# Performance work log

Measured on AMD Instinct MI355X. Metric: run time of the kernel, lower is better.

Reference implementation:

```python
import jax, jax.numpy as jnp
import numpy as np

K = 3          # B-spline order (cubic)
G = 10         # number of spline intervals over [0, 1]
NELY, NELX = 512, 512
WIDTHS = [2, 32, 32, 1]


def _make_grid(in_dim):
    # extended uniform knot vector over [0,1] with K extra knots each side: (in_dim, G+2K+1)
    h = 1.0 / G
    knots = jnp.arange(-K, G + K + 1, dtype=jnp.float32) * h
    return jnp.tile(knots[None, :], (in_dim, 1))


def setup_inputs() -> dict:
    key = jax.random.key(0)
    ks = jax.random.split(key, 1 + 3 * (len(WIDTHS) - 1))
    inp = {"coords": jax.random.uniform(ks[0], (NELY * NELX, 2), dtype=jnp.float32)}
    for l, (i, o) in enumerate(zip(WIDTHS[:-1], WIDTHS[1:])):
        inp[f"grid{l}"] = _make_grid(i)
        inp[f"coef{l}"] = 0.1 * jax.random.normal(ks[1 + 3 * l], (i, o, G + K), dtype=jnp.float32)
        inp[f"sb{l}"] = jax.random.normal(ks[2 + 3 * l], (i, o), dtype=jnp.float32) / np.sqrt(i).astype(np.float32)
        inp[f"sp{l}"] = jnp.ones((i, o), dtype=jnp.float32)
    inp["density_bias"] = jnp.full((1,), np.float32(np.log(0.5 / (1.0 - 0.5 + 1e-8))))
    return inp


def _b_batch(x, grid):
    # Cox-de Boor recursion. x: (B, in), grid: (in, G+2K+1) -> bases (B, in, G+K)
    xe = x[:, :, None]
    v = ((xe >= grid[None, :, :-1]) & (xe < grid[None, :, 1:])).astype(x.dtype)
    for p in range(1, K + 1):
        left = (xe - grid[None, :, : -(p + 1)]) / (grid[None, :, p:-1] - grid[None, :, : -(p + 1)])
        right = (grid[None, :, p + 1:] - xe) / (grid[None, :, p + 1:] - grid[None, :, 1:-p])
        v = left * v[:, :, :-1] + right * v[:, :, 1:]
    return v


def _kan_layer(x, grid, coef, sb, sp):
    # y_out = sum_in [ sb * silu(x) + sp * sum_k B_k(x) * coef_k ]
    B = _b_batch(x, grid)                               # (batch, in, G+K)
    spline = jnp.einsum('bik,iok->bio', B, coef)        # (batch, in, out)
    base = jax.nn.silu(x)                               # (batch, in)
    return jnp.sum(sb[None] * base[:, :, None] + sp[None] * spline, axis=1)


def reference(coords, grid0, coef0, sb0, sp0, grid1, coef1, sb1, sp1,
              grid2, coef2, sb2, sp2, density_bias):
    h = _kan_layer(coords, grid0, coef0, sb0, sp0)
    h = _kan_layer(h, grid1, coef1, sb1, sp1)
    logits = _kan_layer(h, grid2, coef2, sb2, sp2) + density_bias
    return jax.nn.sigmoid(logits).reshape(1, NELY, NELX)
```

## Files before the change

### kernel.cpp

```cpp
#include <hip/hip_runtime.h>
#include <hip/hip_bf16.h>

typedef __hip_bfloat16 bf16;
typedef __fp16 h2v __attribute__((ext_vector_type(2)));
typedef __fp16 half8 __attribute__((ext_vector_type(8)));
typedef float floatx4 __attribute__((ext_vector_type(4)));

#define NPTS (512*512)

#define OFF_BIAS 12
#define OFF_FLAG 13
#define OFF_BF   16
#define NFRAG    50
#define WS_WORDS (16 + NFRAG*64*4)


__device__ __forceinline__ bool sniff_f32(const void* g0) {
    float f = ((const float*)g0)[0];
    return fabsf(f + 0.3f) < 0.01f;
}
__device__ __forceinline__ float ld(const void* p, int i, bool f32) {
    return f32 ? ((const float*)p)[i] : __bfloat162float(((const bf16*)p)[i]);
}
__device__ __forceinline__ unsigned pk_rtn(float a, float b) {
    union { h2v v; unsigned u; } x;
    x.v[0] = (__fp16)a; x.v[1] = (__fp16)b;
    return x.u;
}
__device__ __forceinline__ unsigned pkf16(float a, float b) {
    union { h2v v; unsigned u; } x;
    x.v = __builtin_amdgcn_cvt_pkrtz(a, b);
    return x.u;
}

__device__ float slotval(int layer, int K, int o,
                         const void* c0, const void* sb0, const void* sp0,
                         const void* c1, const void* sb1, const void* sp1,
                         const void* c2, const void* sb2, const void* sp2, bool f32)
{
    int i = K >> 4, s = K & 15;
    if (layer == 2 && o != 0) return 0.0f;
    if (s >= 1 && s <= 13) {
        int m = s - 1;
        if (layer == 0) return ld(c0, (i*32+o)*13 + m, f32) * ld(sp0, i*32+o, f32);
        if (layer == 1) return ld(c1, (i*32+o)*13 + m, f32) * ld(sp1, i*32+o, f32);
        return ld(c2, i*13 + m, f32) * ld(sp2, i, f32);
    }
    if (s == 14) {
        if (layer == 0) return ld(sb0, i*32+o, f32);
        if (layer == 1) return ld(sb1, i*32+o, f32);
        return ld(sb2, i, f32);
    }
    return 0.0f;
}

__global__ __launch_bounds__(256) void kan_prep(
    const void* __restrict__ g0, const void* __restrict__ c0,
    const void* __restrict__ sb0, const void* __restrict__ sp0,
    const void* __restrict__ g1, const void* __restrict__ c1,
    const void* __restrict__ sb1, const void* __restrict__ sp1,
    const void* __restrict__ g2, const void* __restrict__ c2,
    const void* __restrict__ sb2, const void* __restrict__ sp2,
    const void* __restrict__ bias, float* __restrict__ ws)
{
    const bool f32 = sniff_f32(g0);
    int t = blockIdx.x * blockDim.x + threadIdx.x;

    if (t < 16) {
        if (t < 12) {
            int l = t >> 2, j = t & 3;
            const void* g = (l == 0) ? g0 : (l == 1) ? g1 : g2;
            float lo = ld(g, 0, f32), hi = ld(g, 16, f32);
            float ih = 16.0f / (hi - lo);
            float v = (j == 0) ? lo : (j == 1) ? hi
                    : (j == 2) ? ih : (-lo * ih);
            ws[t] = v;
        } else if (t == 12) ws[12] = ld(bias, 0, f32);
        else if (t == 13)   ws[13] = f32 ? 1.0f : 0.0f;
        else                ws[t] = 0.0f;
        return;
    }
    int ft = t - 16;
    if (ft >= NFRAG * 64) return;
    int f = ft >> 6, l = ft & 63, n = l & 15, q = l >> 4;
    int layer, c, nt;
    if (f < 2)       { layer = 0; c = 0;          nt = f; }
    else if (f < 34) { layer = 1; c = (f - 2) >> 1; nt = (f - 2) & 1; }
    else             { layer = 2; c = f - 34;     nt = 0; }
    int o = nt * 16 + n;
    unsigned wv[4];
#pragma unroll
    for (int jp = 0; jp < 4; jp++) {
        int K0 = c * 32 + q * 8 + jp * 2;
        float v0 = slotval(layer, K0,     o, c0,sb0,sp0, c1,sb1,sp1, c2,sb2,sp2, f32);
        float v1 = slotval(layer, K0 + 1, o, c0,sb0,sp0, c1,sb1,sp1, c2,sb2,sp2, f32);
        wv[jp] = pk_rtn(v0, v1);
    }
    uint4 out4; out4.x = wv[0]; out4.y = wv[1]; out4.z = wv[2]; out4.w = wv[3];
    ((uint4*)((unsigned*)ws + OFF_BF))[f * 64 + l] = out4;
}

__device__ __forceinline__ floatx4 mf(uint4 a, uint4 b, floatx4 c)
{
    union { uint4 u; half8 h; } ua, ub;
    ua.u = a; ub.u = b;
    return __builtin_amdgcn_mfma_f32_16x16x32_f16(ua.h, ub.h, c, 0, 0, 0);
}

__device__ __forceinline__ void feat_words(float x, float ngh, float ih,
                                           unsigned* __restrict__ Wd)
{
    float t  = fmaf(x, ih, ngh);
    float fj = floorf(t);
    float u  = t - fj;
    bool inb = (t >= 0.0f) && (t < 16.0f);
    float s6 = inb ? 0.166666667f : 0.0f;
    int j  = (int)fj;
    int jc = min(max(j, 0), 15);
    float u2 = u * u, u3 = u2 * u, om = 1.0f - u;
    float b0 = om * om * om * s6;
    float b1 = (fmaf(3.0f, u3, 4.0f) - 6.0f * u2) * s6;
    float b2 = fmaf(-3.0f, u3, fmaf(3.0f, u2, fmaf(3.0f, u, 1.0f))) * s6;
    float b3 = u3 * s6;
    int m0 = jc - 3;
    if ((unsigned)(m0 + 0) > 12u) b0 = 0.0f;
    if ((unsigned)(m0 + 1) > 12u) b1 = 0.0f;
    if ((unsigned)(m0 + 2) > 12u) b2 = 0.0f;
    if ((unsigned)(m0 + 3) > 12u) b3 = 0.0f;
    int s0 = m0 + 1;
    int w  = ((s0 + 2) >> 1) - 1;
    unsigned A, B, C;
    if (s0 & 1) { A = pkf16(0.0f, b0); B = pkf16(b1, b2); C = pkf16(b3, 0.0f); }
    else        { A = pkf16(b0, b1);   B = pkf16(b2, b3); C = 0u; }
#pragma unroll
    for (int k = 0; k < 7; k++) {
        unsigned v = (w == k) ? A : 0u;
        v = (w == k - 1) ? B : v;
        v = (w == k - 2) ? C : v;
        Wd[k] = v;
    }
    float si = x / (1.0f + __expf(-x));
    Wd[7] = pkf16(si, 0.0f);
}

__device__ __forceinline__ void stage2(unsigned* row, float f0, float f1,
                                       float ngh, float ih)
{
    unsigned Wa[8], Wb[8];
    feat_words(f0, ngh, ih, Wa);
    feat_words(f1, ngh, ih, Wb);
    uint4 v;
    v.x = Wa[0]; v.y = Wa[1]; v.z = Wa[2]; v.w = Wa[3]; *(uint4*)(row + 0)  = v;
    v.x = Wa[4]; v.y = Wa[5]; v.z = Wa[6]; v.w = Wa[7]; *(uint4*)(row + 4)  = v;
    v.x = Wb[0]; v.y = Wb[1]; v.z = Wb[2]; v.w = Wb[3]; *(uint4*)(row + 8)  = v;
    v.x = Wb[4]; v.y = Wb[5]; v.z = Wb[6]; v.w = Wb[7]; *(uint4*)(row + 12) = v;
}

__global__ __launch_bounds__(128, 4) void kan_main(
    const void* __restrict__ coords, const float* __restrict__ ws,
    void* __restrict__ out)
{
    __shared__ __align__(16) unsigned lds[2 * 2560];
    const unsigned* wsu = (const unsigned*)ws;
    const uint4* bfp = (const uint4*)(wsu + OFF_BF);

    int tid = threadIdx.x;
    int l = tid & 63, w = tid >> 6;
    int p = blockIdx.x * 128 + w * 64 + l;

    unsigned* buf0 = lds + w * 2560;
    unsigned* buf1 = buf0 + 1280;
    unsigned* row0 = buf0 + l * 20;
    unsigned* row1 = buf1 + l * 20;

    const bool f32 = (ws[OFF_FLAG] != 0.0f);
    float x0, x1;
    if (f32) {
        float2 c = ((const float2*)coords)[p];
        x0 = c.x; x1 = c.y;
    } else {
        unsigned cc = ((const unsigned*)coords)[p];
        union { unsigned u; float f; } cv;
        cv.u = (cc & 0xffffu) << 16;  x0 = cv.f;
        cv.u = cc & 0xffff0000u;      x1 = cv.f;
    }

    const float iha = ws[2],  ngha = ws[3];
    const float ihb = ws[6],  nghb = ws[7];
    const float ihc = ws[10], nghc = ws[11];

    const int arow = l & 15, aq = (l >> 4) * 4;
    const int aoff = arow * 20 + aq;
    const int drow = (l >> 4) * 4, dcol = l & 15;

    float h[32];

    {
        floatx4 acc[4][2];
#pragma unroll
        for (int mt = 0; mt < 4; mt++)
#pragma unroll
            for (int nt = 0; nt < 2; nt++) acc[mt][nt] = (floatx4)0.0f;

        stage2(row0, x0, x1, ngha, iha);
        uint4 bf0 = bfp[0 * 64 + l], bf1 = bfp[1 * 64 + l];
#pragma unroll
        for (int mt = 0; mt < 4; mt++) {
            uint4 a = *(const uint4*)(buf0 + mt * 320 + aoff);
            acc[mt][0] = mf(a, bf0, acc[mt][0]);
            acc[mt][1] = mf(a, bf1, acc[mt][1]);
        }
#pragma unroll
        for (int mt = 0; mt < 4; mt++)
#pragma unroll
            for (int r = 0; r < 4; r++) {
                int rowi = (16*mt + drow + r) * 20 + dcol;
                buf0[rowi] = __float_as_uint(acc[mt][0][r]);
                buf1[rowi] = __float_as_uint(acc[mt][1][r]);
            }
#pragma unroll
        for (int q = 0; q < 4; q++) {
            uint4 v0 = *(const uint4*)(buf0 + l * 20 + 4 * q);
            h[4*q+0]  = __uint_as_float(v0.x); h[4*q+1]  = __uint_as_float(v0.y);
            h[4*q+2]  = __uint_as_float(v0.z); h[4*q+3]  = __uint_as_float(v0.w);
            uint4 v1 = *(const uint4*)(buf1 + l * 20 + 4 * q);
            h[16+4*q+0] = __uint_as_float(v1.x); h[16+4*q+1] = __uint_as_float(v1.y);
            h[16+4*q+2] = __uint_as_float(v1.z); h[16+4*q+3] = __uint_as_float(v1.w);
        }
    }

    {
        floatx4 acc[4][2];
#pragma unroll
        for (int mt = 0; mt < 4; mt++)
#pragma unroll
            for (int nt = 0; nt < 2; nt++) acc[mt][nt] = (floatx4)0.0f;

        stage2(row0, h[0], h[1], nghb, ihb);
#pragma unroll
        for (int c = 0; c < 16; c++) {
            const unsigned* bc = (c & 1) ? buf1 : buf0;
            unsigned* rn = (c & 1) ? row0 : row1;
            uint4 a[4];
#pragma unroll
            for (int mt = 0; mt < 4; mt++)
                a[mt] = *(const uint4*)(bc + mt * 320 + aoff);
            if (c < 15) stage2(rn, h[2*c+2], h[2*c+3], nghb, ihb);
            uint4 bf0 = bfp[(2 + 2*c) * 64 + l];
            uint4 bf1 = bfp[(3 + 2*c) * 64 + l];
#pragma unroll
            for (int mt = 0; mt < 4; mt++) {
                acc[mt][0] = mf(a[mt], bf0, acc[mt][0]);
                acc[mt][1] = mf(a[mt], bf1, acc[mt][1]);
            }
        }
#pragma unroll
        for (int mt = 0; mt < 4; mt++)
#pragma unroll
            for (int r = 0; r < 4; r++) {
                int rowi = (16*mt + drow + r) * 20 + dcol;
                buf0[rowi] = __float_as_uint(acc[mt][0][r]);
                buf1[rowi] = __float_as_uint(acc[mt][1][r]);
            }
#pragma unroll
        for (int q = 0; q < 4; q++) {
            uint4 v0 = *(const uint4*)(buf0 + l * 20 + 4 * q);
            h[4*q+0]  = __uint_as_float(v0.x); h[4*q+1]  = __uint_as_float(v0.y);
            h[4*q+2]  = __uint_as_float(v0.z); h[4*q+3]  = __uint_as_float(v0.w);
            uint4 v1 = *(const uint4*)(buf1 + l * 20 + 4 * q);
            h[16+4*q+0] = __uint_as_float(v1.x); h[16+4*q+1] = __uint_as_float(v1.y);
            h[16+4*q+2] = __uint_as_float(v1.z); h[16+4*q+3] = __uint_as_float(v1.w);
        }
    }

    {
        floatx4 acc[4];
#pragma unroll
        for (int mt = 0; mt < 4; mt++) acc[mt] = (floatx4)0.0f;

        stage2(row0, h[0], h[1], nghc, ihc);
#pragma unroll
        for (int c = 0; c < 16; c++) {
            const unsigned* bc = (c & 1) ? buf1 : buf0;
            unsigned* rn = (c & 1) ? row0 : row1;
            uint4 a[4];
#pragma unroll
            for (int mt = 0; mt < 4; mt++)
                a[mt] = *(const uint4*)(bc + mt * 320 + aoff);
            if (c < 15) stage2(rn, h[2*c+2], h[2*c+3], nghc, ihc);
            uint4 bf = bfp[(34 + c) * 64 + l];
#pragma unroll
            for (int mt = 0; mt < 4; mt++)
                acc[mt] = mf(a[mt], bf, acc[mt]);
        }
        if (dcol == 0) {
#pragma unroll
            for (int mt = 0; mt < 4; mt++)
#pragma unroll
                for (int r = 0; r < 4; r++)
                    buf0[(16*mt + drow + r) * 20] = __float_as_uint(acc[mt][r]);
        }
        float z = __uint_as_float(buf0[l * 20]);
        float r = 1.0f / (1.0f + __expf(-(z + ws[OFF_BIAS])));
        if (f32) ((float*)out)[p] = r;
        else     ((bf16*)out)[p] = __float2bfloat16(r);
    }
}

extern "C" void kernel_launch(void* const* d_in, const int* in_sizes, int n_in,
                              void* d_out, int out_size, void* d_ws, size_t ws_size,
                              hipStream_t stream)
{
    float* ws = (float*)d_ws;

    kan_prep<<<(16 + NFRAG*64 + 255) / 256, 256, 0, stream>>>(
        d_in[1], d_in[2], d_in[3], d_in[4],
        d_in[5], d_in[6], d_in[7], d_in[8],
        d_in[9], d_in[10], d_in[11], d_in[12],
        d_in[13], ws);

    kan_main<<<NPTS / 128, 128, 0, stream>>>(d_in[0], ws, d_out);
}
```

Measured before the change: 128.9 us.

## Split each point's two input features across two lanes, halving points per wave

Each wave now handles 32 points instead of 64, and two lanes share one point, each computing the B-spline feature words for one of the two input features. Per-lane register state shrinks: fewer accumulators and a 16-entry hidden vector instead of 32. Launch bounds go from 4 to 8 waves per SIMD, LDS per block is halved, and the grid is doubled. This trades more total waves and duplicated sigmoid/output work for lower feature-generation latency per lane and higher occupancy.

Result: no change. 128.9 us (-0.1%).

```diff
diff --git a/kernel.cpp b/kernel.cpp
--- a/kernel.cpp
+++ b/kernel.cpp
@@ -143,167 +143,152 @@
     Wd[7] = pkf16(si, 0.0f);
 }
 
-__device__ __forceinline__ void stage2(unsigned* row, float f0, float f1,
-                                       float ngh, float ih)
-{
-    unsigned Wa[8], Wb[8];
-    feat_words(f0, ngh, ih, Wa);
-    feat_words(f1, ngh, ih, Wb);
+__device__ __forceinline__ void stage1(unsigned* dst, float x, float ngh, float ih)
+{
+    unsigned W[8];
+    feat_words(x, ngh, ih, W);
     uint4 v;
-    v.x = Wa[0]; v.y = Wa[1]; v.z = Wa[2]; v.w = Wa[3]; *(uint4*)(row + 0)  = v;
-    v.x = Wa[4]; v.y = Wa[5]; v.z = Wa[6]; v.w = Wa[7]; *(uint4*)(row + 4)  = v;
-    v.x = Wb[0]; v.y = Wb[1]; v.z = Wb[2]; v.w = Wb[3]; *(uint4*)(row + 8)  = v;
-    v.x = Wb[4]; v.y = Wb[5]; v.z = Wb[6]; v.w = Wb[7]; *(uint4*)(row + 12) = v;
-}
-
-__global__ __launch_bounds__(128, 4) void kan_main(
+    v.x = W[0]; v.y = W[1]; v.z = W[2]; v.w = W[3]; *(uint4*)(dst + 0) = v;
+    v.x = W[4]; v.y = W[5]; v.z = W[6]; v.w = W[7]; *(uint4*)(dst + 4) = v;
+}
+
+__global__ __launch_bounds__(128, 8) void kan_main(
     const void* __restrict__ coords, const float* __restrict__ ws,
     void* __restrict__ out)
 {
-    __shared__ __align__(16) unsigned lds[2 * 2560];
+    __shared__ __align__(16) unsigned lds[2 * 1280];
     const unsigned* wsu = (const unsigned*)ws;
     const uint4* bfp = (const uint4*)(wsu + OFF_BF);
 
     int tid = threadIdx.x;
     int l = tid & 63, w = tid >> 6;
-    int p = blockIdx.x * 128 + w * 64 + l;
-
-    unsigned* buf0 = lds + w * 2560;
-    unsigned* buf1 = buf0 + 1280;
-    unsigned* row0 = buf0 + l * 20;
-    unsigned* row1 = buf1 + l * 20;
+    int r = l & 31, hl = l >> 5;
+    int p = blockIdx.x * 64 + w * 32 + r;
+
+    unsigned* reg0 = lds + w * 1280;
+    unsigned* buf0 = reg0;
+    unsigned* buf1 = reg0 + 640;
+    unsigned* row0 = buf0 + r * 20 + hl * 8;
+    unsigned* row1 = buf1 + r * 20 + hl * 8;
 
     const bool f32 = (ws[OFF_FLAG] != 0.0f);
-    float x0, x1;
+    float x;
     if (f32) {
-        float2 c = ((const float2*)coords)[p];
-        x0 = c.x; x1 = c.y;
+        x = ((const float*)coords)[2 * p + hl];
     } else {
         unsigned cc = ((const unsigned*)coords)[p];
         union { unsigned u; float f; } cv;
-        cv.u = (cc & 0xffffu) << 16;  x0 = cv.f;
-        cv.u = cc & 0xffff0000u;      x1 = cv.f;
+        cv.u = hl ? (cc & 0xffff0000u) : (cc << 16);
+        x = cv.f;
     }
 
     const float iha = ws[2],  ngha = ws[3];
     const float ihb = ws[6],  nghb = ws[7];
     const float ihc = ws[10], nghc = ws[11];
 
-    const int arow = l & 15, aq = (l >> 4) * 4;
-    const int aoff = arow * 20 + aq;
+    const int arow = l & 15;
+    const int aoff = arow * 20 + (l >> 4) * 4;
     const int drow = (l >> 4) * 4, dcol = l & 15;
-
-    float h[32];
+    const int wword = 16 * (dcol & 1) + (dcol >> 1);
+
+    float hv[16];
 
     {
-        floatx4 acc[4][2];
-#pragma unroll
-        for (int mt = 0; mt < 4; mt++)
+        floatx4 acc[2][2];
+#pragma unroll
+        for (int mt = 0; mt < 2; mt++)
 #pragma unroll
             for (int nt = 0; nt < 2; nt++) acc[mt][nt] = (floatx4)0.0f;
 
-        stage2(row0, x0, x1, ngha, iha);
+        stage1(row0, x, ngha, iha);
         uint4 bf0 = bfp[0 * 64 + l], bf1 = bfp[1 * 64 + l];
 #pragma unroll
-        for (int mt = 0; mt < 4; mt++) {
+        for (int mt = 0; mt < 2; mt++) {
             uint4 a = *(const uint4*)(buf0 + mt * 320 + aoff);
             acc[mt][0] = mf(a, bf0, acc[mt][0]);
             acc[mt][1] = mf(a, bf1, acc[mt][1]);
         }
 #pragma unroll
-        for (int mt = 0; mt < 4; mt++)
-#pragma unroll
-            for (int r = 0; r < 4; r++) {
-                int rowi = (16*mt + drow + r) * 20 + dcol;
-                buf0[rowi] = __float_as_uint(acc[mt][0][r]);
-                buf1[rowi] = __float_as_uint(acc[mt][1][r]);
-            }
-#pragma unroll
-        for (int q = 0; q < 4; q++) {
-            uint4 v0 = *(const uint4*)(buf0 + l * 20 + 4 * q);
-            h[4*q+0]  = __uint_as_float(v0.x); h[4*q+1]  = __uint_as_float(v0.y);
-            h[4*q+2]  = __uint_as_float(v0.z); h[4*q+3]  = __uint_as_float(v0.w);
-            uint4 v1 = *(const uint4*)(buf1 + l * 20 + 4 * q);
-            h[16+4*q+0] = __uint_as_float(v1.x); h[16+4*q+1] = __uint_as_float(v1.y);
-            h[16+4*q+2] = __uint_as_float(v1.z); h[16+4*q+3] = __uint_as_float(v1.w);
+        for (int mt = 0; mt < 2; mt++)
+#pragma unroll
+            for (int nt = 0; nt < 2; nt++)
+#pragma unroll
+                for (int rg = 0; rg < 4; rg++)
+                    reg0[(16*mt + drow + rg) * 36 + wword + 8*nt] =
+                        __float_as_uint(acc[mt][nt][rg]);
+#pragma unroll
+        for (int jq = 0; jq < 4; jq++) {
+            uint4 v = *(const uint4*)(reg0 + r * 36 + 16 * hl + 4 * jq);
+            hv[4*jq+0] = __uint_as_float(v.x); hv[4*jq+1] = __uint_as_float(v.y);
+            hv[4*jq+2] = __uint_as_float(v.z); hv[4*jq+3] = __uint_as_float(v.w);
         }
     }
 
     {
-        floatx4 acc[4][2];
-#pragma unroll
-        for (int mt = 0; mt < 4; mt++)
+        floatx4 acc[2][2];
+#pragma unroll
+        for (int mt = 0; mt < 2; mt++)
 #pragma unroll
             for (int nt = 0; nt < 2; nt++) acc[mt][nt] = (floatx4)0.0f;
 
-        stage2(row0, h[0], h[1], nghb, ihb);
+        stage1(row0, hv[0], nghb, ihb);
 #pragma unroll
         for (int c = 0; c < 16; c++) {
             const unsigned* bc = (c & 1) ? buf1 : buf0;
-            unsigned* rn = (c & 1) ? row0 : row1;
-            uint4 a[4];
-#pragma unroll
-            for (int mt = 0; mt < 4; mt++)
-                a[mt] = *(const uint4*)(bc + mt * 320 + aoff);
-            if (c < 15) stage2(rn, h[2*c+2], h[2*c+3], nghb, ihb);
+            uint4 a0 = *(const uint4*)(bc + aoff);
+            uint4 a1 = *(const uint4*)(bc + 320 + aoff);
+            if (c < 15) stage1((c & 1) ? row0 : row1, hv[c + 1], nghb, ihb);
             uint4 bf0 = bfp[(2 + 2*c) * 64 + l];
             uint4 bf1 = bfp[(3 + 2*c) * 64 + l];
-#pragma unroll
-            for (int mt = 0; mt < 4; mt++) {
-                acc[mt][0] = mf(a[mt], bf0, acc[mt][0]);
-                acc[mt][1] = mf(a[mt], bf1, acc[mt][1]);
-            }
-        }
-#pragma unroll
-        for (int mt = 0; mt < 4; mt++)
-#pragma unroll
-            for (int r = 0; r < 4; r++) {
-                int rowi = (16*mt + drow + r) * 20 + dcol;
-                buf0[rowi] = __float_as_uint(acc[mt][0][r]);
-                buf1[rowi] = __float_as_uint(acc[mt][1][r]);
-            }
-#pragma unroll
-        for (int q = 0; q < 4; q++) {
-            uint4 v0 = *(const uint4*)(buf0 + l * 20 + 4 * q);
-            h[4*q+0]  = __uint_as_float(v0.x); h[4*q+1]  = __uint_as_float(v0.y);
-            h[4*q+2]  = __uint_as_float(v0.z); h[4*q+3]  = __uint_as_float(v0.w);
-            uint4 v1 = *(const uint4*)(buf1 + l * 20 + 4 * q);
-            h[16+4*q+0] = __uint_as_float(v1.x); h[16+4*q+1] = __uint_as_float(v1.y);
-            h[16+4*q+2] = __uint_as_float(v1.z); h[16+4*q+3] = __uint_as_float(v1.w);
+            acc[0][0] = mf(a0, bf0, acc[0][0]);
+            acc[0][1] = mf(a0, bf1, acc[0][1]);
+            acc[1][0] = mf(a1, bf0, acc[1][0]);
+            acc[1][1] = mf(a1, bf1, acc[1][1]);
+        }
+#pragma unroll
+        for (int mt = 0; mt < 2; mt++)
+#pragma unroll
+            for (int nt = 0; nt < 2; nt++)
+#pragma unroll
+                for (int rg = 0; rg < 4; rg++)
+                    reg0[(16*mt + drow + rg) * 36 + wword + 8*nt] =
+                        __float_as_uint(acc[mt][nt][rg]);
+#pragma unroll
+        for (int jq = 0; jq < 4; jq++) {
+            uint4 v = *(const uint4*)(reg0 + r * 36 + 16 * hl + 4 * jq);
+            hv[4*jq+0] = __uint_as_float(v.x); hv[4*jq+1] = __uint_as_float(v.y);
+            hv[4*jq+2] = __uint_as_float(v.z); hv[4*jq+3] = __uint_as_float(v.w);
         }
     }
 
     {
-        floatx4 acc[4];
-#pragma unroll
-        for (int mt = 0; mt < 4; mt++) acc[mt] = (floatx4)0.0f;
-
-        stage2(row0, h[0], h[1], nghc, ihc);
+        floatx4 acc2[2];
+        acc2[0] = (floatx4)0.0f; acc2[1] = (floatx4)0.0f;
+
+        stage1(row0, hv[0], nghc, ihc);
 #pragma unroll
         for (int c = 0; c < 16; c++) {
             const unsigned* bc = (c & 1) ? buf1 : buf0;
-            unsigned* rn = (c & 1) ? row0 : row1;
-            uint4 a[4];
-#pragma unroll
-            for (int mt = 0; mt < 4; mt++)
-                a[mt] = *(const uint4*)(bc + mt * 320 + aoff);
-            if (c < 15) stage2(rn, h[2*c+2], h[2*c+3], nghc, ihc);
+            uint4 a0 = *(const uint4*)(bc + aoff);
+            uint4 a1 = *(const uint4*)(bc + 320 + aoff);
+            if (c < 15) stage1((c & 1) ? row0 : row1, hv[c + 1], nghc, ihc);
             uint4 bf = bfp[(34 + c) * 64 + l];
-#pragma unroll
-            for (int mt = 0; mt < 4; mt++)
-                acc[mt] = mf(a[mt], bf, acc[mt]);
+            acc2[0] = mf(a0, bf, acc2[0]);
+            acc2[1] = mf(a1, bf, acc2[1]);
         }
         if (dcol == 0) {
 #pragma unroll
-            for (int mt = 0; mt < 4; mt++)
-#pragma unroll
-                for (int r = 0; r < 4; r++)
-                    buf0[(16*mt + drow + r) * 20] = __float_as_uint(acc[mt][r]);
-        }
-        float z = __uint_as_float(buf0[l * 20]);
-        float r = 1.0f / (1.0f + __expf(-(z + ws[OFF_BIAS])));
-        if (f32) ((float*)out)[p] = r;
-        else     ((bf16*)out)[p] = __float2bfloat16(r);
+            for (int mt = 0; mt < 2; mt++)
+#pragma unroll
+                for (int rg = 0; rg < 4; rg++)
+                    reg0[(16*mt + drow + rg) * 36] = __float_as_uint(acc2[mt][rg]);
+        }
+        float z = __uint_as_float(reg0[r * 36]);
+        float res = 1.0f / (1.0f + __expf(-(z + ws[OFF_BIAS])));
+        if (hl == 0) {
+            if (f32) ((float*)out)[p] = res;
+            else     ((bf16*)out)[p] = __float2bfloat16(res);
+        }
     }
 }
 
@@ -319,5 +304,5 @@
         d_in[9], d_in[10], d_in[11], d_in[12],
         d_in[13], ws);
 
-    kan_main<<<NPTS / 128, 128, 0, stream>>>(d_in[0], ws, d_out);
-}
+    kan_main<<<NPTS / 64, 128, 0, stream>>>(d_in[0], ws, d_out);
+}
```
